# Performance work log

Hardware: AMD Instinct MI355X
Metric: run time of the kernel (lower is better)

Reference implementation:

```python
import jax, jax.numpy as jnp
import numpy as np

B, T, C = 8, 2048, 1024
NEG = -1e30  # stand-in for -inf in the stable-softmax running max


def setup_inputs() -> dict:
    key = jax.random.key(0)
    ks = jax.random.split(key, 5)
    x = jax.random.normal(ks[0], (B, T, C), dtype=jnp.float32)
    scales = jnp.arange(C, dtype=jnp.float32) / C  # matches init_weight()
    Wk = jax.random.normal(ks[1], (C, C), dtype=jnp.float32) * 0.02
    Wv = jax.random.normal(ks[2], (C, C), dtype=jnp.float32) * 0.02
    Wr = jax.random.normal(ks[3], (C, C), dtype=jnp.float32) * 0.02
    Wo = jax.random.normal(ks[4], (C, C), dtype=jnp.float32) * 0.02
    return {
        'x': x,
        'w': scales, 'u': scales,
        'mix_k': scales, 'mix_v': scales, 'mix_r': scales,
        'Wk': Wk, 'Wv': Wv, 'Wr': Wr, 'Wo': Wo,
    }


def wkv(w, u, k, v):
    # Numerically-stable RWKV WKV recurrence. k, v: [B, T, C]; w, u: [C]
    w_exp = -jnp.exp(w)  # per-channel log-decay (negative)
    p0 = jnp.zeros(k.shape[::2], k.dtype)      # [B, C] numerator state
    q0 = jnp.zeros(k.shape[::2], k.dtype)      # [B, C] denominator state
    o0 = jnp.full(k.shape[::2], NEG, k.dtype)  # [B, C] running max (log-space)

    def step(carry, kv_t):
        p, q, o = carry
        k_t, v_t = kv_t  # each [B, C]
        uk = u + k_t
        no = jnp.maximum(o, uk)
        A = jnp.exp(o - no)
        Bc = jnp.exp(uk - no)
        out = (A * p + Bc * v_t) / (A * q + Bc)
        wo = w_exp + o
        no2 = jnp.maximum(wo, k_t)
        A2 = jnp.exp(wo - no2)
        B2 = jnp.exp(k_t - no2)
        return (A2 * p + B2 * v_t, A2 * q + B2, no2), out

    kT = jnp.swapaxes(k, 0, 1)  # [T, B, C]
    vT = jnp.swapaxes(v, 0, 1)
    _, outs = jax.lax.scan(step, (p0, q0, o0), (kT, vT))
    return jnp.swapaxes(outs, 0, 1)  # [B, T, C]


def reference(x, w, u, mix_k, mix_v, mix_r, Wk, Wv, Wr, Wo):
    # time_shift: ZeroPad2d((0,0,1,-1)) => shift sequence right by one, zero-pad front
    x_prev = jnp.pad(x, ((0, 0), (1, 0), (0, 0)))[:, :-1]
    # torch.lerp(start=x_prev, end=x, weight=mix)
    xk = x_prev + mix_k * (x - x_prev)
    xv = x_prev + mix_v * (x - x_prev)
    xr = x_prev + mix_r * (x - x_prev)
    k = jnp.einsum('btc,dc->btd', xk, Wk)
    v = jnp.einsum('btc,dc->btd', xv, Wv)
    sr = jax.nn.sigmoid(jnp.einsum('btc,dc->btd', xr, Wr))
    rwkv = sr * wkv(w, u, k, v)
    return jnp.einsum('btc,dc->btd', rwkv, Wo)
```

## Files before the change

### kernel.cpp

```cpp
#include <hip/hip_runtime.h>
#include <hip/hip_bf16.h>
#include <stdint.h>

#define Bb   8
#define Tt   2048
#define Cdim 1024
#define BT   16384
#define SLAB ((size_t)BT * Cdim)

#define NC   32
#define LCH  64
#define CSUB 32

typedef __attribute__((ext_vector_type(4))) float f32x4;
typedef __attribute__((ext_vector_type(8))) short bf16x8;

__device__ inline short f2bs(float f) {
    union { __hip_bfloat16 h; short s; } u;
    u.h = __float2bfloat16(f);
    return u.s;
}
__device__ inline float bs2f(short s) {
    union { short s; __hip_bfloat16 h; } u;
    u.s = s;
    return __bfloat162float(u.h);
}

#define GLOAD_LDS16(g, l) __builtin_amdgcn_global_load_lds( \
    (const __attribute__((address_space(1))) void*)(g),     \
    (__attribute__((address_space(3))) void*)(l), 16, 0, 0)

#define SBAR()      __builtin_amdgcn_s_barrier()

__global__ __launch_bounds__(256) void prep_x(
    const float* __restrict__ x,
    const float* __restrict__ mk,
    const float* __restrict__ mv,
    const float* __restrict__ mr,
    short* __restrict__ xmix)
{
    int idx = blockIdx.x * 256 + threadIdx.x;
    int c8  = idx & (Cdim / 8 - 1);
    int m   = idx >> 7;
    int c0  = c8 << 3;
    int t   = m & (Tt - 1);

    float xs[8], ps[8];
    const float4* xp = (const float4*)(x + (size_t)m * Cdim + c0);
    float4 xa = xp[0], xb = xp[1];
    xs[0]=xa.x; xs[1]=xa.y; xs[2]=xa.z; xs[3]=xa.w;
    xs[4]=xb.x; xs[5]=xb.y; xs[6]=xb.z; xs[7]=xb.w;
    if (t != 0) {
        const float4* pp = (const float4*)(x + (size_t)(m - 1) * Cdim + c0);
        float4 pa = pp[0], pb = pp[1];
        ps[0]=pa.x; ps[1]=pa.y; ps[2]=pa.z; ps[3]=pa.w;
        ps[4]=pb.x; ps[5]=pb.y; ps[6]=pb.z; ps[7]=pb.w;
    } else {
        #pragma unroll
        for (int j = 0; j < 8; ++j) ps[j] = 0.f;
    }

    const float* mixes[3] = {mk, mv, mr};
    #pragma unroll
    for (int z = 0; z < 3; ++z) {
        const float4* mp = (const float4*)(mixes[z] + c0);
        float4 ma = mp[0], mb = mp[1];
        float mm[8];
        mm[0]=ma.x; mm[1]=ma.y; mm[2]=ma.z; mm[3]=ma.w;
        mm[4]=mb.x; mm[5]=mb.y; mm[6]=mb.z; mm[7]=mb.w;
        bf16x8 o;
        #pragma unroll
        for (int j = 0; j < 8; ++j)
            o[j] = f2bs(ps[j] + mm[j] * (xs[j] - ps[j]));
        *(bf16x8*)(xmix + (size_t)z * SLAB + (size_t)m * Cdim + c0) = o;
    }
}

__global__ __launch_bounds__(256) void prep_w(
    const float* __restrict__ Wk, const float* __restrict__ Wv,
    const float* __restrict__ Wr, const float* __restrict__ Wo,
    short* __restrict__ wbf)
{
    int idx = blockIdx.x * 256 + threadIdx.x;
    int z   = idx >> 17;
    int r   = idx & (Cdim * Cdim / 8 - 1);
    const float* src = (z == 0) ? Wk : (z == 1) ? Wv : (z == 2) ? Wr : Wo;
    const float4* sp = (const float4*)(src + (size_t)r * 8);
    float4 a = sp[0], b = sp[1];
    float v[8] = {a.x, a.y, a.z, a.w, b.x, b.y, b.z, b.w};
    bf16x8 o;
    #pragma unroll
    for (int j = 0; j < 8; ++j) o[j] = f2bs(v[j]);
    *(bf16x8*)(wbf + (size_t)z * Cdim * Cdim + (size_t)r * 8) = o;
}

template<int FUSED>
__global__ __launch_bounds__(512, 2) void gemm256(
    const short* __restrict__ Abase,
    const short* __restrict__ Wbase,
    void* __restrict__ o0, void* __restrict__ o1, void* __restrict__ o2)
{
    __shared__ __align__(16) char lds[131072];

    const int tid  = threadIdx.x;
    const int lane = tid & 63;
    const int wv   = tid >> 6;
    const int wm   = wv >> 2, wn = wv & 3;
    const int NT   = Cdim / 64;

    int orig = blockIdx.y * (FUSED ? 12 : 4) + blockIdx.x;
    int xcd  = orig & 7;
    int s    = orig >> 3;
    int z, nt, yt;
    if (FUSED) {
        z  = s >> 5;
        int rem = s & 31;
        nt = rem & 3;
        yt = xcd * 8 + (rem >> 2);
    } else {
        z  = 0;
        nt = s & 3;
        yt = xcd * 8 + (s >> 2);
    }

    const short* A  = Abase + (size_t)z * SLAB;
    const short* Bm = Wbase + (size_t)z * Cdim * Cdim;
    const int m0 = yt * 256;
    const int n0 = nt * 256;

    f32x4 acc[8][4] = {};

    const int lm = lane & 15, lq = lane >> 4, lb7 = lane & 7;
    int ck[2];
    #pragma unroll
    for (int ks = 0; ks < 2; ++ks) ck[ks] = (((ks * 4 + lq) ^ lb7) << 4);
    int aoff[8];
    #pragma unroll
    for (int i = 0; i < 8; ++i) aoff[i] = (i * 16 + lm) * 128;
    int boff[4];
    #pragma unroll
    for (int j = 0; j < 4; ++j) boff[j] = ((wn & 1) * 64 + j * 16 + lm) * 128;
    const int aReg = wm << 14;
    const int bReg = 32768 + ((wn >> 1) << 14);

    const int rlo  = tid >> 3;
    const int clog = (tid & 7) ^ (rlo & 7);
    auto STAGE = [&](int tt, int part) {
        const short* mat = (part < 2) ? A : Bm;
        int rb = ((part < 2) ? m0 : n0) + ((part & 1) << 7);
        const short* g0 = mat + (size_t)(rb + rlo)      * Cdim + (tt << 6) + (clog << 3);
        const short* g1 = mat + (size_t)(rb + 64 + rlo) * Cdim + (tt << 6) + (clog << 3);
        char* l = lds + ((tt & 1) << 16) + (part << 14) + tid * 16;
        GLOAD_LDS16(g0, l);
        GLOAD_LDS16(g1, l + 8192);
    };

    STAGE(0, 0); STAGE(0, 1); STAGE(0, 2); STAGE(0, 3);
    STAGE(1, 0); STAGE(1, 1);
    asm volatile("s_waitcnt vmcnt(4)" ::: "memory");
    SBAR();

    bf16x8 a0[4][2], a4[4][2], b01[2][2], b23[2][2];

    #pragma unroll 1
    for (int kt = 0; kt < NT; ++kt) {
        const char* base = lds + ((kt & 1) << 16);

        #pragma unroll
        for (int i = 0; i < 4; ++i)
            #pragma unroll
            for (int ks = 0; ks < 2; ++ks)
                a0[i][ks] = *(const bf16x8*)(base + aReg + aoff[i] + ck[ks]);
        #pragma unroll
        for (int j = 0; j < 2; ++j)
            #pragma unroll
            for (int ks = 0; ks < 2; ++ks)
                b01[j][ks] = *(const bf16x8*)(base + bReg + boff[j] + ck[ks]);
        #pragma unroll
        for (int i = 0; i < 4; ++i)
            #pragma unroll
            for (int ks = 0; ks < 2; ++ks)
                a4[i][ks] = *(const bf16x8*)(base + aReg + aoff[i + 4] + ck[ks]);
        if (kt + 1 < NT) STAGE(kt + 1, 2);
        __builtin_amdgcn_s_setprio(1);
        #pragma unroll
        for (int ks = 0; ks < 2; ++ks)
            #pragma unroll
            for (int i = 0; i < 4; ++i)
                #pragma unroll
                for (int j = 0; j < 2; ++j)
                    acc[i][j] = __builtin_amdgcn_mfma_f32_16x16x32_bf16(
                        a0[i][ks], b01[j][ks], acc[i][j], 0, 0, 0);
        __builtin_amdgcn_s_setprio(0);
        SBAR();

        #pragma unroll
        for (int j = 0; j < 2; ++j)
            #pragma unroll
            for (int ks = 0; ks < 2; ++ks)
                b23[j][ks] = *(const bf16x8*)(base + bReg + boff[j + 2] + ck[ks]);
        if (kt + 1 < NT) STAGE(kt + 1, 3);
        __builtin_amdgcn_s_setprio(1);
        #pragma unroll
        for (int ks = 0; ks < 2; ++ks)
            #pragma unroll
            for (int i = 0; i < 4; ++i)
                #pragma unroll
                for (int j = 0; j < 2; ++j)
                    acc[i + 4][j] = __builtin_amdgcn_mfma_f32_16x16x32_bf16(
                        a4[i][ks], b01[j][ks], acc[i + 4][j], 0, 0, 0);
        __builtin_amdgcn_s_setprio(0);
        SBAR();

        if (kt + 2 < NT) STAGE(kt + 2, 0);
        __builtin_amdgcn_s_setprio(1);
        #pragma unroll
        for (int ks = 0; ks < 2; ++ks)
            #pragma unroll
            for (int i = 0; i < 4; ++i)
                #pragma unroll
                for (int j = 0; j < 2; ++j)
                    acc[i + 4][j + 2] = __builtin_amdgcn_mfma_f32_16x16x32_bf16(
                        a4[i][ks], b23[j][ks], acc[i + 4][j + 2], 0, 0, 0);
        __builtin_amdgcn_s_setprio(0);
        SBAR();

        if (kt + 2 < NT) STAGE(kt + 2, 1);
        __builtin_amdgcn_s_setprio(1);
        #pragma unroll
        for (int ks = 0; ks < 2; ++ks)
            #pragma unroll
            for (int i = 0; i < 4; ++i)
                #pragma unroll
                for (int j = 0; j < 2; ++j)
                    acc[i][j + 2] = __builtin_amdgcn_mfma_f32_16x16x32_bf16(
                        a0[i][ks], b23[j][ks], acc[i][j + 2], 0, 0, 0);
        __builtin_amdgcn_s_setprio(0);
        if      (kt + 2 < NT) { asm volatile("s_waitcnt vmcnt(4)" ::: "memory"); }
        else if (kt + 1 < NT) { asm volatile("s_waitcnt vmcnt(0)" ::: "memory"); }
        SBAR();
    }

    int col0 = n0 + wn * 64 + lm;
    int row0 = m0 + wm * 128 + (lq << 2);
    short* outb = 0;
    if (FUSED) outb = (short*)((z == 0) ? o0 : (z == 1) ? o1 : o2);
    #pragma unroll
    for (int i = 0; i < 8; ++i) {
        #pragma unroll
        for (int j = 0; j < 4; ++j) {
            #pragma unroll
            for (int r = 0; r < 4; ++r) {
                int row = row0 + i * 16 + r;
                int cc  = col0 + j * 16;
                float vvv = acc[i][j][r];
                if (FUSED) {
                    if (z == 2) vvv = 1.f / (1.f + __expf(-vvv));
                    outb[(size_t)row * Cdim + cc] = f2bs(vvv);
                } else {
                    ((float*)o0)[(size_t)row * Cdim + cc] = vvv;
                }
            }
        }
    }
}

__global__ __launch_bounds__(1024) void wkv_chunked(
    const short* __restrict__ kb, const short* __restrict__ vb,
    const short* __restrict__ srb,
    const float* __restrict__ w, const float* __restrict__ u,
    short* __restrict__ rwkv)
{
    __shared__ float sp[NC][CSUB];
    __shared__ float sq[NC][CSUB];
    __shared__ float so[NC][CSUB];

    int tid = threadIdx.x;
    int cl  = tid & (CSUB - 1);
    int ch  = tid >> 5;
    int b   = blockIdx.x >> 5;
    int cg  = blockIdx.x & 31;
    int c   = cg * CSUB + cl;

    float wexp = -__expf(w[c]);
    float uu   = u[c];
    size_t coff = (size_t)b * Tt * Cdim + (size_t)(ch * LCH) * Cdim + c;

    float p = 0.f, q = 0.f, o = -1e30f;
    #pragma unroll 8
    for (int t = 0; t < LCH; ++t) {
        size_t off = coff + (size_t)t * Cdim;
        float kt = bs2f(kb[off]);
        float vt = bs2f(vb[off]);
        float wo  = wexp + o;
        float no  = fmaxf(wo, kt);
        float A   = __expf(wo - no);
        float B2  = __expf(kt - no);
        p = A * p + B2 * vt;
        q = A * q + B2;
        o = no;
    }
    sp[ch][cl] = p; sq[ch][cl] = q; so[ch][cl] = o;
    __syncthreads();

    if (tid < CSUB) {
        float Ld = wexp * (float)LCH;
        float cp = 0.f, cq = 0.f, co = -1e30f;
        for (int j = 0; j < NC; ++j) {
            float lp = sp[j][tid], lq = sq[j][tid], lo = so[j][tid];
            sp[j][tid] = cp; sq[j][tid] = cq; so[j][tid] = co;
            float od = co + Ld;
            float no = fmaxf(od, lo);
            float A  = __expf(od - no);
            float B2 = __expf(lo - no);
            cp = A * cp + B2 * lp;
            cq = A * cq + B2 * lq;
            co = no;
        }
    }
    __syncthreads();

    p = sp[ch][cl]; q = sq[ch][cl]; o = so[ch][cl];
    #pragma unroll 8
    for (int t = 0; t < LCH; ++t) {
        size_t off = coff + (size_t)t * Cdim;
        float kt = bs2f(kb[off]);
        float vt = bs2f(vb[off]);
        float sr = bs2f(srb[off]);

        float uk  = uu + kt;
        float no  = fmaxf(o, uk);
        float Aa  = __expf(o - no);
        float Bc  = __expf(uk - no);
        float out = (Aa * p + Bc * vt) / (Aa * q + Bc);

        float wo  = wexp + o;
        float no2 = fmaxf(wo, kt);
        float A2  = __expf(wo - no2);
        float B2  = __expf(kt - no2);
        p = A2 * p + B2 * vt;
        q = A2 * q + B2;
        o = no2;

        rwkv[off] = f2bs(sr * out);
    }
}

extern "C" void kernel_launch(void* const* d_in, const int* in_sizes, int n_in,
                              void* d_out, int out_size, void* d_ws, size_t ws_size,
                              hipStream_t stream)
{
    const float* x    = (const float*)d_in[0];
    const float* w    = (const float*)d_in[1];
    const float* u    = (const float*)d_in[2];
    const float* mixk = (const float*)d_in[3];
    const float* mixv = (const float*)d_in[4];
    const float* mixr = (const float*)d_in[5];
    const float* Wk   = (const float*)d_in[6];
    const float* Wv   = (const float*)d_in[7];
    const float* Wr   = (const float*)d_in[8];
    const float* Wo   = (const float*)d_in[9];

    char* ws = (char*)d_ws;
    short* xmix = (short*)ws;
    short* wbf  = (short*)(ws + 3 * SLAB * 2);
    short* rbuf = (short*)(ws + 3 * SLAB * 2 + (size_t)4 * Cdim * Cdim * 2);
    short* rwkv = (short*)ws;
    short* kbuf = (short*)d_out;
    short* vbuf = kbuf + SLAB;

    prep_x<<<BT * Cdim / 8 / 256, 256, 0, stream>>>(x, mixk, mixv, mixr, xmix);
    prep_w<<<4 * Cdim * Cdim / 8 / 256, 256, 0, stream>>>(Wk, Wv, Wr, Wo, wbf);

    dim3 gf(12, BT / 256);
    gemm256<1><<<gf, 512, 0, stream>>>(xmix, wbf, kbuf, vbuf, rbuf);

    wkv_chunked<<<Bb * (Cdim / CSUB), 1024, 0, stream>>>(kbuf, vbuf, rbuf, w, u, rwkv);

    dim3 go(Cdim / 256, BT / 256);
    gemm256<0><<<go, 512, 0, stream>>>(rwkv, wbf + 3 * (size_t)Cdim * Cdim,
                                       (float*)d_out, nullptr, nullptr);
}
```

Baseline: 240.9 us.

## Merge prep kernels, coarsen GEMM barrier phases, interleave k/v buffers

```diff
diff --git a/kernel.cpp b/kernel.cpp
--- a/kernel.cpp
+++ b/kernel.cpp
@@ -32,73 +32,73 @@
 
 #define SBAR()      __builtin_amdgcn_s_barrier()
 
-__global__ __launch_bounds__(256) void prep_x(
+__global__ __launch_bounds__(256) void prep_all(
     const float* __restrict__ x,
     const float* __restrict__ mk,
     const float* __restrict__ mv,
     const float* __restrict__ mr,
-    short* __restrict__ xmix)
-{
-    int idx = blockIdx.x * 256 + threadIdx.x;
-    int c8  = idx & (Cdim / 8 - 1);
-    int m   = idx >> 7;
-    int c0  = c8 << 3;
-    int t   = m & (Tt - 1);
-
-    float xs[8], ps[8];
-    const float4* xp = (const float4*)(x + (size_t)m * Cdim + c0);
-    float4 xa = xp[0], xb = xp[1];
-    xs[0]=xa.x; xs[1]=xa.y; xs[2]=xa.z; xs[3]=xa.w;
-    xs[4]=xb.x; xs[5]=xb.y; xs[6]=xb.z; xs[7]=xb.w;
-    if (t != 0) {
-        const float4* pp = (const float4*)(x + (size_t)(m - 1) * Cdim + c0);
-        float4 pa = pp[0], pb = pp[1];
-        ps[0]=pa.x; ps[1]=pa.y; ps[2]=pa.z; ps[3]=pa.w;
-        ps[4]=pb.x; ps[5]=pb.y; ps[6]=pb.z; ps[7]=pb.w;
-    } else {
-        #pragma unroll
-        for (int j = 0; j < 8; ++j) ps[j] = 0.f;
-    }
-
-    const float* mixes[3] = {mk, mv, mr};
-    #pragma unroll
-    for (int z = 0; z < 3; ++z) {
-        const float4* mp = (const float4*)(mixes[z] + c0);
-        float4 ma = mp[0], mb = mp[1];
-        float mm[8];
-        mm[0]=ma.x; mm[1]=ma.y; mm[2]=ma.z; mm[3]=ma.w;
-        mm[4]=mb.x; mm[5]=mb.y; mm[6]=mb.z; mm[7]=mb.w;
-        bf16x8 o;
-        #pragma unroll
-        for (int j = 0; j < 8; ++j)
-            o[j] = f2bs(ps[j] + mm[j] * (xs[j] - ps[j]));
-        *(bf16x8*)(xmix + (size_t)z * SLAB + (size_t)m * Cdim + c0) = o;
-    }
-}
-
-__global__ __launch_bounds__(256) void prep_w(
     const float* __restrict__ Wk, const float* __restrict__ Wv,
     const float* __restrict__ Wr, const float* __restrict__ Wo,
+    short* __restrict__ xmix,
     short* __restrict__ wbf)
 {
-    int idx = blockIdx.x * 256 + threadIdx.x;
-    int z   = idx >> 17;
-    int r   = idx & (Cdim * Cdim / 8 - 1);
-    const float* src = (z == 0) ? Wk : (z == 1) ? Wv : (z == 2) ? Wr : Wo;
-    const float4* sp = (const float4*)(src + (size_t)r * 8);
-    float4 a = sp[0], b = sp[1];
-    float v[8] = {a.x, a.y, a.z, a.w, b.x, b.y, b.z, b.w};
-    bf16x8 o;
-    #pragma unroll
-    for (int j = 0; j < 8; ++j) o[j] = f2bs(v[j]);
-    *(bf16x8*)(wbf + (size_t)z * Cdim * Cdim + (size_t)r * 8) = o;
+    int bid = blockIdx.x;
+    if (bid < 8192) {
+        int idx = bid * 256 + threadIdx.x;
+        int c8  = idx & (Cdim / 8 - 1);
+        int m   = idx >> 7;
+        int c0  = c8 << 3;
+        int t   = m & (Tt - 1);
+
+        float xs[8], ps[8];
+        const float4* xp = (const float4*)(x + (size_t)m * Cdim + c0);
+        float4 xa = xp[0], xb = xp[1];
+        xs[0]=xa.x; xs[1]=xa.y; xs[2]=xa.z; xs[3]=xa.w;
+        xs[4]=xb.x; xs[5]=xb.y; xs[6]=xb.z; xs[7]=xb.w;
+        if (t != 0) {
+            const float4* pp = (const float4*)(x + (size_t)(m - 1) * Cdim + c0);
+            float4 pa = pp[0], pb = pp[1];
+            ps[0]=pa.x; ps[1]=pa.y; ps[2]=pa.z; ps[3]=pa.w;
+            ps[4]=pb.x; ps[5]=pb.y; ps[6]=pb.z; ps[7]=pb.w;
+        } else {
+            #pragma unroll
+            for (int j = 0; j < 8; ++j) ps[j] = 0.f;
+        }
+
+        const float* mixes[3] = {mk, mv, mr};
+        #pragma unroll
+        for (int z = 0; z < 3; ++z) {
+            const float4* mp = (const float4*)(mixes[z] + c0);
+            float4 ma = mp[0], mb = mp[1];
+            float mm[8];
+            mm[0]=ma.x; mm[1]=ma.y; mm[2]=ma.z; mm[3]=ma.w;
+            mm[4]=mb.x; mm[5]=mb.y; mm[6]=mb.z; mm[7]=mb.w;
+            bf16x8 o;
+            #pragma unroll
+            for (int j = 0; j < 8; ++j)
+                o[j] = f2bs(ps[j] + mm[j] * (xs[j] - ps[j]));
+            *(bf16x8*)(xmix + (size_t)z * SLAB + (size_t)m * Cdim + c0) = o;
+        }
+    } else {
+        int idx = (bid - 8192) * 256 + threadIdx.x;
+        int z   = idx >> 17;
+        int r   = idx & (Cdim * Cdim / 8 - 1);
+        const float* src = (z == 0) ? Wk : (z == 1) ? Wv : (z == 2) ? Wr : Wo;
+        const float4* sp = (const float4*)(src + (size_t)r * 8);
+        float4 a = sp[0], b = sp[1];
+        float v[8] = {a.x, a.y, a.z, a.w, b.x, b.y, b.z, b.w};
+        bf16x8 o;
+        #pragma unroll
+        for (int j = 0; j < 8; ++j) o[j] = f2bs(v[j]);
+        *(bf16x8*)(wbf + (size_t)z * Cdim * Cdim + (size_t)r * 8) = o;
+    }
 }
 
 template<int FUSED>
 __global__ __launch_bounds__(512, 2) void gemm256(
     const short* __restrict__ Abase,
     const short* __restrict__ Wbase,
-    void* __restrict__ o0, void* __restrict__ o1, void* __restrict__ o2)
+    void* __restrict__ o0, void* __restrict__ o1)
 {
     __shared__ __align__(16) char lds[131072];
 
@@ -181,7 +181,12 @@
             #pragma unroll
             for (int ks = 0; ks < 2; ++ks)
                 a4[i][ks] = *(const bf16x8*)(base + aReg + aoff[i + 4] + ck[ks]);
-        if (kt + 1 < NT) STAGE(kt + 1, 2);
+        #pragma unroll
+        for (int j = 0; j < 2; ++j)
+            #pragma unroll
+            for (int ks = 0; ks < 2; ++ks)
+                b23[j][ks] = *(const bf16x8*)(base + bReg + boff[j + 2] + ck[ks]);
+        if (kt + 1 < NT) { STAGE(kt + 1, 2); STAGE(kt + 1, 3); }
         __builtin_amdgcn_s_setprio(1);
         #pragma unroll
         for (int ks = 0; ks < 2; ++ks)
@@ -191,16 +196,6 @@
                 for (int j = 0; j < 2; ++j)
                     acc[i][j] = __builtin_amdgcn_mfma_f32_16x16x32_bf16(
                         a0[i][ks], b01[j][ks], acc[i][j], 0, 0, 0);
-        __builtin_amdgcn_s_setprio(0);
-        SBAR();
-
-        #pragma unroll
-        for (int j = 0; j < 2; ++j)
-            #pragma unroll
-            for (int ks = 0; ks < 2; ++ks)
-                b23[j][ks] = *(const bf16x8*)(base + bReg + boff[j + 2] + ck[ks]);
-        if (kt + 1 < NT) STAGE(kt + 1, 3);
-        __builtin_amdgcn_s_setprio(1);
         #pragma unroll
         for (int ks = 0; ks < 2; ++ks)
             #pragma unroll
@@ -212,7 +207,7 @@
         __builtin_amdgcn_s_setprio(0);
         SBAR();
 
-        if (kt + 2 < NT) STAGE(kt + 2, 0);
+        if (kt + 2 < NT) { STAGE(kt + 2, 0); STAGE(kt + 2, 1); }
         __builtin_amdgcn_s_setprio(1);
         #pragma unroll
         for (int ks = 0; ks < 2; ++ks)
@@ -222,11 +217,6 @@
                 for (int j = 0; j < 2; ++j)
                     acc[i + 4][j + 2] = __builtin_amdgcn_mfma_f32_16x16x32_bf16(
                         a4[i][ks], b23[j][ks], acc[i + 4][j + 2], 0, 0, 0);
-        __builtin_amdgcn_s_setprio(0);
-        SBAR();
-
-        if (kt + 2 < NT) STAGE(kt + 2, 1);
-        __builtin_amdgcn_s_setprio(1);
         #pragma unroll
         for (int ks = 0; ks < 2; ++ks)
             #pragma unroll
@@ -243,8 +233,6 @@
 
     int col0 = n0 + wn * 64 + lm;
     int row0 = m0 + wm * 128 + (lq << 2);
-    short* outb = 0;
-    if (FUSED) outb = (short*)((z == 0) ? o0 : (z == 1) ? o1 : o2);
     #pragma unroll
     for (int i = 0; i < 8; ++i) {
         #pragma unroll
@@ -255,8 +243,12 @@
                 int cc  = col0 + j * 16;
                 float vvv = acc[i][j][r];
                 if (FUSED) {
-                    if (z == 2) vvv = 1.f / (1.f + __expf(-vvv));
-                    outb[(size_t)row * Cdim + cc] = f2bs(vvv);
+                    if (z == 2) {
+                        ((short*)o1)[(size_t)row * Cdim + cc] =
+                            f2bs(1.f / (1.f + __expf(-vvv)));
+                    } else {
+                        ((short*)o0)[((size_t)row * Cdim + cc) * 2 + z] = f2bs(vvv);
+                    }
                 } else {
                     ((float*)o0)[(size_t)row * Cdim + cc] = vvv;
                 }
@@ -266,8 +258,7 @@
 }
 
 __global__ __launch_bounds__(1024) void wkv_chunked(
-    const short* __restrict__ kb, const short* __restrict__ vb,
-    const short* __restrict__ srb,
+    const int* __restrict__ kv, const short* __restrict__ srb,
     const float* __restrict__ w, const float* __restrict__ u,
     short* __restrict__ rwkv)
 {
@@ -290,8 +281,9 @@
     #pragma unroll 8
     for (int t = 0; t < LCH; ++t) {
         size_t off = coff + (size_t)t * Cdim;
-        float kt = bs2f(kb[off]);
-        float vt = bs2f(vb[off]);
+        int pk = kv[off];
+        float kt = bs2f((short)(pk & 0xffff));
+        float vt = bs2f((short)((unsigned)pk >> 16));
         float wo  = wexp + o;
         float no  = fmaxf(wo, kt);
         float A   = __expf(wo - no);
@@ -324,8 +316,9 @@
     #pragma unroll 8
     for (int t = 0; t < LCH; ++t) {
         size_t off = coff + (size_t)t * Cdim;
-        float kt = bs2f(kb[off]);
-        float vt = bs2f(vb[off]);
+        int pk = kv[off];
+        float kt = bs2f((short)(pk & 0xffff));
+        float vt = bs2f((short)((unsigned)pk >> 16));
         float sr = bs2f(srb[off]);
 
         float uk  = uu + kt;
@@ -366,18 +359,17 @@
     short* wbf  = (short*)(ws + 3 * SLAB * 2);
     short* rbuf = (short*)(ws + 3 * SLAB * 2 + (size_t)4 * Cdim * Cdim * 2);
     short* rwkv = (short*)ws;
-    short* kbuf = (short*)d_out;
-    short* vbuf = kbuf + SLAB;
-
-    prep_x<<<BT * Cdim / 8 / 256, 256, 0, stream>>>(x, mixk, mixv, mixr, xmix);
-    prep_w<<<4 * Cdim * Cdim / 8 / 256, 256, 0, stream>>>(Wk, Wv, Wr, Wo, wbf);
+    int*   kvbf = (int*)d_out;
+
+    prep_all<<<8192 + 2048, 256, 0, stream>>>(x, mixk, mixv, mixr,
+                                              Wk, Wv, Wr, Wo, xmix, wbf);
 
     dim3 gf(12, BT / 256);
-    gemm256<1><<<gf, 512, 0, stream>>>(xmix, wbf, kbuf, vbuf, rbuf);
-
-    wkv_chunked<<<Bb * (Cdim / CSUB), 1024, 0, stream>>>(kbuf, vbuf, rbuf, w, u, rwkv);
+    gemm256<1><<<gf, 512, 0, stream>>>(xmix, wbf, kvbf, rbuf);
+
+    wkv_chunked<<<Bb * (Cdim / CSUB), 1024, 0, stream>>>(kvbf, rbuf, w, u, rwkv);
 
     dim3 go(Cdim / 256, BT / 256);
     gemm256<0><<<go, 512, 0, stream>>>(rwkv, wbf + 3 * (size_t)Cdim * Cdim,
-                                       (float*)d_out, nullptr, nullptr);
-}
+                                       (float*)d_out, nullptr);
+}
```

Measured after the change: 235.5 us. 2.3% less time.
